# Kernel tuning notes

Hardware: AMD Instinct MI355X
Metric: run time of the kernel (lower is better)

The kernel has to match this reference:

```python
import jax, jax.numpy as jnp
import numpy as np

D_MODEL = 1024
NUM_HEADS = 16
D_K = D_MODEL // NUM_HEADS


def setup_inputs() -> dict:
    key = jax.random.key(0)
    ks = jax.random.split(key, 9)
    B, S = 4, 2048
    scale = 1.0 / np.sqrt(D_MODEL)
    x = jax.random.normal(ks[0], (B, S, D_MODEL), dtype=jnp.float32)
    Wq = jax.random.uniform(ks[1], (D_MODEL, D_MODEL), jnp.float32, -scale, scale)
    Wk = jax.random.uniform(ks[2], (D_MODEL, D_MODEL), jnp.float32, -scale, scale)
    Wv = jax.random.uniform(ks[3], (D_MODEL, D_MODEL), jnp.float32, -scale, scale)
    Wo = jax.random.uniform(ks[4], (D_MODEL, D_MODEL), jnp.float32, -scale, scale)
    bq = jax.random.uniform(ks[5], (D_MODEL,), jnp.float32, -scale, scale)
    bk = jax.random.uniform(ks[6], (D_MODEL,), jnp.float32, -scale, scale)
    bv = jax.random.uniform(ks[7], (D_MODEL,), jnp.float32, -scale, scale)
    bo = jax.random.uniform(ks[8], (D_MODEL,), jnp.float32, -scale, scale)
    return {"x": x, "Wq": Wq, "bq": bq, "Wk": Wk, "bk": bk, "Wv": Wv, "bv": bv, "Wo": Wo, "bo": bo}


def _split_heads(t, B, S):
    # (B, S, D) -> (B, H, S, d_k)
    return t.reshape(B, S, NUM_HEADS, D_K).transpose(0, 2, 1, 3)


def reference(x, Wq, bq, Wk, bk, Wv, bv, Wo, bo):
    B, S, D = x.shape
    Q = _split_heads(x @ Wq + bq, B, S)
    K = _split_heads(x @ Wk + bk, B, S)
    V = _split_heads(x @ Wv + bv, B, S)
    # scores: (B, H, S, S) — naive materialization, faithful to original
    scores = jnp.einsum('bhqd,bhkd->bhqk', Q, K) / np.sqrt(D_K)
    weights = jax.nn.softmax(scores.astype(jnp.float32), axis=-1).astype(scores.dtype)
    # dropout p=0.0 in eval mode -> identity
    attn = jnp.einsum('bhqk,bhkd->bhqd', weights, V)
    attn = attn.transpose(0, 2, 1, 3).reshape(B, S, D)
    return attn @ Wo + bo
```

## Files before the change

### kernel.cpp

```cpp
#include <hip/hip_runtime.h>
#include <hip/hip_bf16.h>
#include <stdint.h>
#include <string.h>

using u16 = unsigned short;
typedef __attribute__((ext_vector_type(8))) short short8;
typedef __attribute__((ext_vector_type(4))) float f32x4;

__device__ __forceinline__ u16 f2bf(float f) {
  union { float f; unsigned int u; } x; x.f = f;
  unsigned int u = x.u;
  return (u16)((u + 0x7fffu + ((u >> 16) & 1u)) >> 16);
}
__device__ __forceinline__ unsigned int pk_bf16(float a, float b) {
  float2 t; t.x = a; t.y = b;
  __hip_bfloat162 h = __float22bfloat162_rn(t);
  unsigned int u; memcpy(&u, &h, 4);
  return u;
}
__device__ __forceinline__ void gl_lds16(const u16* g, u16* l) {
  __builtin_amdgcn_global_load_lds((const __attribute__((address_space(1))) void*)g,
                                   (__attribute__((address_space(3))) void*)l, 16, 0, 0);
}

__global__ void __launch_bounds__(256) conv_x(
    const float* __restrict__ in, u16* __restrict__ out, int n4) {
  const int t = blockIdx.x * 256 + threadIdx.x;
  if (t >= n4) return;
  const float4 v = ((const float4*)in)[t];
  uint2 o;
  o.x = pk_bf16(v.x, v.y);
  o.y = pk_bf16(v.z, v.w);
  ((uint2*)out)[t] = o;
}

__global__ void __launch_bounds__(256) transpose_w(
    const float* __restrict__ W0, const float* __restrict__ W1,
    const float* __restrict__ W2, const float* __restrict__ W3,
    u16* __restrict__ Wt) {
  __shared__ alignas(16) u16 t[64][65];
  const int z = blockIdx.z;
  const float* in = (z == 0) ? W0 : (z == 1) ? W1 : (z == 2) ? W2 : W3;
  u16* out = Wt + (size_t)z * 1024 * 1024;
  const int tx = threadIdx.x & 63, ty = threadIdx.x >> 6;
  const int r0 = blockIdx.y * 64, c0 = blockIdx.x * 64;
#pragma unroll
  for (int rr = ty; rr < 64; rr += 4) t[rr][tx] = f2bf(in[(size_t)(r0 + rr) * 1024 + c0 + tx]);
  __syncthreads();
#pragma unroll
  for (int rr = ty; rr < 64; rr += 4) out[(size_t)(c0 + rr) * 1024 + r0 + tx] = t[tx][rr];
}

__device__ __forceinline__ void gemm_core(
    const u16* __restrict__ A, const u16* __restrict__ Bt,
    u16* As, u16* Bs, int m0, int n0, int K, f32x4 (&acc)[4][4]) {
  const int tid = threadIdx.x;
  const int wave = tid >> 6, lane = tid & 63;
  const int quad = lane >> 4, l16 = lane & 15;
  const int wr = wave >> 1, wc = wave & 1;
  const int lr = lane >> 2, lc = (lane & 3) * 8;
  for (int k0 = 0; k0 < K; k0 += 32) {
    __syncthreads();
#pragma unroll
    for (int t = 0; t < 2; ++t) {
      const int c = wave + t * 4;
      gl_lds16(A  + (size_t)(m0 + c * 16 + lr) * K + k0 + lc, &As[c * 16 * 32]);
      gl_lds16(Bt + (size_t)(n0 + c * 16 + lr) * K + k0 + lc, &Bs[c * 16 * 32]);
    }
    __syncthreads();
    short8 af[4], bfr[4];
#pragma unroll
    for (int i = 0; i < 4; ++i)
      af[i] = *(const short8*)&As[(wr * 64 + i * 16 + l16) * 32 + quad * 8];
#pragma unroll
    for (int j = 0; j < 4; ++j)
      bfr[j] = *(const short8*)&Bs[(wc * 64 + j * 16 + l16) * 32 + quad * 8];
#pragma unroll
    for (int i = 0; i < 4; ++i)
#pragma unroll
      for (int j = 0; j < 4; ++j)
        acc[i][j] = __builtin_amdgcn_mfma_f32_16x16x32_bf16(af[i], bfr[j], acc[i][j], 0, 0, 0);
  }
}

__global__ void __launch_bounds__(256) gemm_qkv(
    const u16* __restrict__ A, const u16* __restrict__ Wt,
    const float* __restrict__ bq, const float* __restrict__ bk, const float* __restrict__ bv,
    u16* __restrict__ Qb, u16* __restrict__ Kb, u16* __restrict__ Vtb) {
  __shared__ alignas(16) u16 As[128 * 32];
  __shared__ alignas(16) u16 Bs[128 * 32];
  const int tsel = blockIdx.x >> 3;
  const int n0 = (blockIdx.x & 7) * 128;
  const int m0 = blockIdx.y * 128;
  const u16* Bt = Wt + (size_t)tsel * 1048576;
  const float* bias = (tsel == 0) ? bq : (tsel == 1) ? bk : bv;

  f32x4 acc[4][4];
#pragma unroll
  for (int i = 0; i < 4; ++i)
#pragma unroll
    for (int j = 0; j < 4; ++j) acc[i][j] = (f32x4){0.f, 0.f, 0.f, 0.f};

  gemm_core(A, Bt, As, Bs, m0, n0, 1024, acc);

  const int tid = threadIdx.x;
  const int wave = tid >> 6, lane = tid & 63;
  const int quad = lane >> 4, l16 = lane & 15;
  const int wr = wave >> 1, wc = wave & 1;

  if (tsel < 2) {
    u16* C = tsel ? Kb : Qb;
#pragma unroll
    for (int j = 0; j < 4; ++j) {
      const int n = n0 + wc * 64 + j * 16 + l16;
      const float bvf = bias[n];
      const int h = n >> 6, d = n & 63;
#pragma unroll
      for (int i = 0; i < 4; ++i) {
        const int mbase = m0 + wr * 64 + i * 16 + quad * 4;
#pragma unroll
        for (int r = 0; r < 4; ++r) {
          const int m = mbase + r;
          const int b = m >> 11, s = m & 2047;
          C[((((size_t)b * 16 + h) * 2048) + s) * 64 + d] = f2bf(acc[i][j][r] + bvf);
        }
      }
    }
  } else {
#pragma unroll
    for (int j = 0; j < 4; ++j) {
      const int n = n0 + wc * 64 + j * 16 + l16;
      const float bvf = bias[n];
      const int h = n >> 6, d = n & 63;
#pragma unroll
      for (int i = 0; i < 4; ++i) {
        const int mbase = m0 + wr * 64 + i * 16 + quad * 4;
        const int b = mbase >> 11, s = mbase & 2047;
        uint2 o;
        o.x = pk_bf16(acc[i][j][0] + bvf, acc[i][j][1] + bvf);
        o.y = pk_bf16(acc[i][j][2] + bvf, acc[i][j][3] + bvf);
        *(uint2*)&Vtb[(((size_t)b * 16 + h) * 64 + d) * 2048 + s] = o;
      }
    }
  }
}

__global__ void __launch_bounds__(256) gemm_out(
    const u16* __restrict__ A, const u16* __restrict__ Bt,
    const float* __restrict__ bias, float* __restrict__ C, int N) {
  __shared__ alignas(16) u16 As[128 * 32];
  __shared__ alignas(16) u16 Bs[128 * 32];
  const int m0 = blockIdx.y * 128;
  const int n0 = blockIdx.x * 128;
  f32x4 acc[4][4];
#pragma unroll
  for (int i = 0; i < 4; ++i)
#pragma unroll
    for (int j = 0; j < 4; ++j) acc[i][j] = (f32x4){0.f, 0.f, 0.f, 0.f};

  gemm_core(A, Bt, As, Bs, m0, n0, 1024, acc);

  const int tid = threadIdx.x;
  const int wave = tid >> 6, lane = tid & 63;
  const int quad = lane >> 4, l16 = lane & 15;
  const int wr = wave >> 1, wc = wave & 1;
#pragma unroll
  for (int j = 0; j < 4; ++j) {
    const int n = n0 + wc * 64 + j * 16 + l16;
    const float bvf = bias[n];
#pragma unroll
    for (int i = 0; i < 4; ++i) {
      const int mbase = m0 + wr * 64 + i * 16 + quad * 4;
#pragma unroll
      for (int r = 0; r < 4; ++r)
        C[(size_t)(mbase + r) * N + n] = acc[i][j][r] + bvf;
    }
  }
}

__global__ void __launch_bounds__(256) flash_attn(
    const u16* __restrict__ Q, const u16* __restrict__ Kp,
    const u16* __restrict__ Vt, u16* __restrict__ Aout) {
  __shared__ alignas(16) u16 Qs[64 * 64];
  __shared__ alignas(16) u16 Ks[64 * 64];
  __shared__ alignas(16) u16 Vs[64 * 64];
  __shared__ alignas(16) u16 Pq[4][16 * 72];

  const int tid = threadIdx.x;
  const int wave = tid >> 6;
  const int lane = tid & 63;
  const int quad = lane >> 4;
  const int l16 = lane & 15;
  const int bh = blockIdx.y;
  const int q0 = blockIdx.x * 64;
  const int b = bh >> 4, h = bh & 15;

  const u16* Qg = Q + (size_t)bh * 2048 * 64;
  const u16* Kg = Kp + (size_t)bh * 2048 * 64;
  const u16* Vg = Vt + (size_t)bh * 64 * 2048;

  const int lr8 = lane >> 3;
  const int cbg = ((lane & 7) ^ lr8) * 8;

#pragma unroll
  for (int t = 0; t < 2; ++t) {
    const int c = wave * 2 + t;
    gl_lds16(Qg + (size_t)(q0 + c * 8 + lr8) * 64 + cbg, &Qs[c * 8 * 64]);
  }

  f32x4 oacc[4];
#pragma unroll
  for (int t = 0; t < 4; ++t) oacc[t] = (f32x4){0.f, 0.f, 0.f, 0.f};
  float l = 0.f;
  const float cexp = 0.125f * 1.44269504088896340736f;
  u16* Pw = &Pq[wave][0];
  const int sw = (l16 & 7) * 8;

  for (int kt = 0; kt < 32; ++kt) {
    const int s0 = kt * 64;
    __syncthreads();
#pragma unroll
    for (int t = 0; t < 2; ++t) {
      const int c = wave * 2 + t;
      gl_lds16(Kg + (size_t)(s0 + c * 8 + lr8) * 64 + cbg, &Ks[c * 8 * 64]);
      gl_lds16(Vg + (size_t)(c * 8 + lr8) * 2048 + s0 + cbg, &Vs[c * 8 * 64]);
    }
    __syncthreads();

    f32x4 sacc[4];
#pragma unroll
    for (int t = 0; t < 4; ++t) sacc[t] = (f32x4){0.f, 0.f, 0.f, 0.f};
#pragma unroll
    for (int ks = 0; ks < 2; ++ks) {
      const short8 bqf = *(const short8*)&Qs[(wave * 16 + l16) * 64 + (((ks * 4 + quad) * 8) ^ sw)];
#pragma unroll
      for (int t = 0; t < 4; ++t) {
        const short8 akf = *(const short8*)&Ks[(t * 16 + l16) * 64 + (((ks * 4 + quad) * 8) ^ sw)];
        sacc[t] = __builtin_amdgcn_mfma_f32_16x16x32_bf16(akf, bqf, sacc[t], 0, 0, 0);
      }
    }

    float rs = 0.f;
#pragma unroll
    for (int t = 0; t < 4; ++t) {
      const float p0 = exp2f(sacc[t][0] * cexp);
      const float p1 = exp2f(sacc[t][1] * cexp);
      const float p2 = exp2f(sacc[t][2] * cexp);
      const float p3 = exp2f(sacc[t][3] * cexp);
      rs += (p0 + p1) + (p2 + p3);
      uint2 pk;
      pk.x = pk_bf16(p0, p1);
      pk.y = pk_bf16(p2, p3);
      *(uint2*)&Pw[l16 * 72 + t * 16 + quad * 4] = pk;
    }
    rs += __shfl_xor(rs, 16);
    rs += __shfl_xor(rs, 32);
    l += rs;

    asm volatile("s_waitcnt lgkmcnt(0)" ::: "memory");

#pragma unroll
    for (int ks = 0; ks < 2; ++ks) {
      const short8 bpf = *(const short8*)&Pw[l16 * 72 + ks * 32 + quad * 8];
#pragma unroll
      for (int t = 0; t < 4; ++t) {
        const short8 avf = *(const short8*)&Vs[(t * 16 + l16) * 64 + (((ks * 4 + quad) * 8) ^ sw)];
        oacc[t] = __builtin_amdgcn_mfma_f32_16x16x32_bf16(avf, bpf, oacc[t], 0, 0, 0);
      }
    }
  }

  const float inv = 1.0f / l;
  const int qrow = q0 + wave * 16 + l16;
  const size_t base = ((size_t)b * 2048 + qrow) * 1024 + h * 64 + quad * 4;
#pragma unroll
  for (int t = 0; t < 4; ++t) {
    uint2 o;
    o.x = pk_bf16(oacc[t][0] * inv, oacc[t][1] * inv);
    o.y = pk_bf16(oacc[t][2] * inv, oacc[t][3] * inv);
    *(uint2*)&Aout[base + t * 16] = o;
  }
}

extern "C" void kernel_launch(void* const* d_in, const int* in_sizes, int n_in,
                              void* d_out, int out_size, void* d_ws, size_t ws_size,
                              hipStream_t stream) {
  (void)in_sizes; (void)n_in; (void)out_size; (void)ws_size;
  const float* x  = (const float*)d_in[0];
  const float* Wq = (const float*)d_in[1];
  const float* bq = (const float*)d_in[2];
  const float* Wk = (const float*)d_in[3];
  const float* bk = (const float*)d_in[4];
  const float* Wv = (const float*)d_in[5];
  const float* bv = (const float*)d_in[6];
  const float* Wo = (const float*)d_in[7];
  const float* bo = (const float*)d_in[8];
  float* out = (float*)d_out;

  u16* ws = (u16*)d_ws;
  const size_t SZ = (size_t)4 * 16 * 2048 * 64;
  u16* xb   = ws;
  u16* Qb   = ws + SZ;
  u16* Kb   = ws + 2 * SZ;
  u16* Vtb  = ws + 3 * SZ;
  u16* Wt   = ws + 4 * SZ;
  u16* Attn = ws;

  dim3 blk(256);
  conv_x<<<dim3(8192), blk, 0, stream>>>(x, xb, 2097152);
  transpose_w<<<dim3(16, 16, 4), blk, 0, stream>>>(Wq, Wk, Wv, Wo, Wt);
  gemm_qkv<<<dim3(24, 64), blk, 0, stream>>>(xb, Wt, bq, bk, bv, Qb, Kb, Vtb);
  flash_attn<<<dim3(32, 64), blk, 0, stream>>>(Qb, Kb, Vtb, Attn);
  gemm_out<<<dim3(8, 64), blk, 0, stream>>>(Attn, Wt + (size_t)3 * 1048576, bo, out, 1024);
}
```

Measured before the change: 352.3 us.

## Keep P in registers via 16x16x16 MFMA, hoist Q fragments, defer row-sum reduction

Removes the per-wave LDS round-trip for the softmax probability tile by feeding the packed bf16 P values directly as the B operand of 16x16x16 bf16 MFMAs, whose register layout matches the QK^T accumulator output. Q fragments are loaded once into registers (reusing the K buffer for staging) instead of being reread from LDS every key tile. The row-sum cross-lane shuffles are moved out of the loop to the end. In exchange, twice as many smaller MFMA instructions are issued for PV, and there is an inline-asm fallback with manual nops if the builtin is missing.

Result: slower. 367.5 us (+4.3%).

```diff
diff --git a/kernel.cpp b/kernel.cpp
--- a/kernel.cpp
+++ b/kernel.cpp
@@ -5,6 +5,7 @@
 
 using u16 = unsigned short;
 typedef __attribute__((ext_vector_type(8))) short short8;
+typedef __attribute__((ext_vector_type(4))) short short4v;
 typedef __attribute__((ext_vector_type(4))) float f32x4;
 
 __device__ __forceinline__ u16 f2bf(float f) {
@@ -181,10 +182,8 @@
 __global__ void __launch_bounds__(256) flash_attn(
     const u16* __restrict__ Q, const u16* __restrict__ Kp,
     const u16* __restrict__ Vt, u16* __restrict__ Aout) {
-  __shared__ alignas(16) u16 Qs[64 * 64];
   __shared__ alignas(16) u16 Ks[64 * 64];
   __shared__ alignas(16) u16 Vs[64 * 64];
-  __shared__ alignas(16) u16 Pq[4][16 * 72];
 
   const int tid = threadIdx.x;
   const int wave = tid >> 6;
@@ -201,20 +200,25 @@
 
   const int lr8 = lane >> 3;
   const int cbg = ((lane & 7) ^ lr8) * 8;
+  const int sw = (l16 & 7) * 8;
+  const int swq = l16 & 7;
 
 #pragma unroll
   for (int t = 0; t < 2; ++t) {
     const int c = wave * 2 + t;
-    gl_lds16(Qg + (size_t)(q0 + c * 8 + lr8) * 64 + cbg, &Qs[c * 8 * 64]);
-  }
+    gl_lds16(Qg + (size_t)(q0 + c * 8 + lr8) * 64 + cbg, &Ks[c * 8 * 64]);
+  }
+  __syncthreads();
+  short8 qf[2];
+#pragma unroll
+  for (int ks = 0; ks < 2; ++ks)
+    qf[ks] = *(const short8*)&Ks[(wave * 16 + l16) * 64 + (((ks * 4 + quad) * 8) ^ sw)];
 
   f32x4 oacc[4];
 #pragma unroll
   for (int t = 0; t < 4; ++t) oacc[t] = (f32x4){0.f, 0.f, 0.f, 0.f};
   float l = 0.f;
   const float cexp = 0.125f * 1.44269504088896340736f;
-  u16* Pw = &Pq[wave][0];
-  const int sw = (l16 & 7) * 8;
 
   for (int kt = 0; kt < 32; ++kt) {
     const int s0 = kt * 64;
@@ -232,44 +236,52 @@
     for (int t = 0; t < 4; ++t) sacc[t] = (f32x4){0.f, 0.f, 0.f, 0.f};
 #pragma unroll
     for (int ks = 0; ks < 2; ++ks) {
-      const short8 bqf = *(const short8*)&Qs[(wave * 16 + l16) * 64 + (((ks * 4 + quad) * 8) ^ sw)];
 #pragma unroll
       for (int t = 0; t < 4; ++t) {
         const short8 akf = *(const short8*)&Ks[(t * 16 + l16) * 64 + (((ks * 4 + quad) * 8) ^ sw)];
-        sacc[t] = __builtin_amdgcn_mfma_f32_16x16x32_bf16(akf, bqf, sacc[t], 0, 0, 0);
+        sacc[t] = __builtin_amdgcn_mfma_f32_16x16x32_bf16(akf, qf[ks], sacc[t], 0, 0, 0);
       }
     }
 
-    float rs = 0.f;
+    short4v pk[4];
 #pragma unroll
     for (int t = 0; t < 4; ++t) {
       const float p0 = exp2f(sacc[t][0] * cexp);
       const float p1 = exp2f(sacc[t][1] * cexp);
       const float p2 = exp2f(sacc[t][2] * cexp);
       const float p3 = exp2f(sacc[t][3] * cexp);
-      rs += (p0 + p1) + (p2 + p3);
-      uint2 pk;
-      pk.x = pk_bf16(p0, p1);
-      pk.y = pk_bf16(p2, p3);
-      *(uint2*)&Pw[l16 * 72 + t * 16 + quad * 4] = pk;
-    }
-    rs += __shfl_xor(rs, 16);
-    rs += __shfl_xor(rs, 32);
-    l += rs;
-
-    asm volatile("s_waitcnt lgkmcnt(0)" ::: "memory");
-
-#pragma unroll
-    for (int ks = 0; ks < 2; ++ks) {
-      const short8 bpf = *(const short8*)&Pw[l16 * 72 + ks * 32 + quad * 8];
-#pragma unroll
-      for (int t = 0; t < 4; ++t) {
-        const short8 avf = *(const short8*)&Vs[(t * 16 + l16) * 64 + (((ks * 4 + quad) * 8) ^ sw)];
-        oacc[t] = __builtin_amdgcn_mfma_f32_16x16x32_bf16(avf, bpf, oacc[t], 0, 0, 0);
+      l += (p0 + p1) + (p2 + p3);
+      uint2 u;
+      u.x = pk_bf16(p0, p1);
+      u.y = pk_bf16(p2, p3);
+      memcpy(&pk[t], &u, 8);
+    }
+
+#pragma unroll
+    for (int t = 0; t < 4; ++t) {
+#pragma unroll
+      for (int t2 = 0; t2 < 4; ++t2) {
+        const short4v vf = *(const short4v*)&Vs[(t2 * 16 + l16) * 64 +
+                                               (((2 * t + (quad >> 1)) ^ swq) * 8) + (quad & 1) * 4];
+#if __has_builtin(__builtin_amdgcn_mfma_f32_16x16x16bf16_1k)
+        oacc[t2] = __builtin_amdgcn_mfma_f32_16x16x16bf16_1k(vf, pk[t], oacc[t2], 0, 0, 0);
+#else
+        asm volatile("s_nop 2\n\tv_mfma_f32_16x16x16_bf16 %0, %1, %2, %0"
+                     : "+v"(oacc[t2]) : "v"(vf), "v"(pk[t]));
+#endif
       }
     }
-  }
-
+#if !__has_builtin(__builtin_amdgcn_mfma_f32_16x16x16bf16_1k)
+    asm volatile("s_nop 7" ::);
+#endif
+  }
+
+#if !__has_builtin(__builtin_amdgcn_mfma_f32_16x16x16bf16_1k)
+  asm volatile("s_nop 7\n\ts_nop 7\n\ts_nop 3" ::);
+#endif
+
+  l += __shfl_xor(l, 16);
+  l += __shfl_xor(l, 32);
   const float inv = 1.0f / l;
   const int qrow = q0 + wave * 16 + l16;
   const size_t base = ((size_t)b * 2048 + qrow) * 1024 + h * 64 + quad * 4;
```
